# Kernel optimization log

Measured on AMD Instinct MI355X. Metric: run time of the kernel, lower is better.

The kernel has to match this reference:

```python
import jax, jax.numpy as jnp
import numpy as np
import math

D = 1024      # d_model
DC = 256      # d_cache
DL = DC // 4  # d_layer
K = 64        # num_slots
NL = 8        # num_layers
N = NL * K    # cache slots (L*K)
P = 16        # num_patterns
H = 16        # num_heads
B, S = 8, 1024
F = 4 * D

def _linear(x, w, b):
    return jnp.matmul(x, w.T) + b

def _ln(x, g, b):
    m = jnp.mean(x, -1, keepdims=True)
    v = jnp.mean((x - m) ** 2, -1, keepdims=True)
    return (x - m) * jax.lax.rsqrt(v + 1e-5) * g + b

def _mha(q, k, v, wqkv, bqkv, wo, bo, nh):
    # torch nn.MultiheadAttention (batch_first, eval/no-dropout)
    d = q.shape[-1]; dh = d // nh
    wq, wk, wv = jnp.split(wqkv, 3, axis=0)
    bq, bk, bv = jnp.split(bqkv, 3, axis=0)
    qh = _linear(q, wq, bq).reshape(q.shape[0], q.shape[1], nh, dh)
    kh = _linear(k, wk, bk).reshape(k.shape[0], k.shape[1], nh, dh)
    vh = _linear(v, wv, bv).reshape(v.shape[0], v.shape[1], nh, dh)
    s = jnp.einsum('bqhd,bkhd->bhqk', qh, kh) * (1.0 / math.sqrt(dh))
    a = jax.nn.softmax(s, axis=-1)
    o = jnp.einsum('bhqk,bkhd->bqhd', a, vh).reshape(q.shape[0], q.shape[1], d)
    return _linear(o, wo, bo)

def _forward(x, cache, slot_embeddings, layer_ids, gumbel_u, layer_embed,
             attn_wqkv, attn_bqkv, attn_wo, attn_bo,
             pat_wqkv, pat_bqkv, pat_wo, pat_bo, pattern_queries,
             ffn_w1, ffn_b1, ffn_w2, ffn_b2,
             n1_g, n1_b, n2_g, n2_b,
             gate_w, gate_b, sel_w, sel_b, sq_w, sq_b, sk_w, sk_b, an_w, an_b,
             dec_w, dec_b, cq_w, cq_b, ck_w, ck_b, cv_w, cv_b, fg_w, fg_b):
    b, s, d = x.shape
    # --- read_cache: cross-attention from tokens to [B,N,DC] cache slots ---
    cid = jnp.concatenate([cache, jnp.broadcast_to(layer_ids[None], (b,) + layer_ids.shape)], axis=-1)  # [B,N,DC+DL]
    q = _linear(x, cq_w, cq_b)                    # [B,S,DC]
    kk = _linear(cid, ck_w, ck_b)                 # [B,N,DC]
    vv = _linear(cid, cv_w, cv_b)                 # [B,N,DC]
    sc = jnp.einsum('bsd,bnd->bsn', q, kk) * (1.0 / math.sqrt(DC))
    attn = jax.nn.softmax(sc, axis=-1)
    ctx = jnp.einsum('bsn,bnd->bsd', attn, vv)    # [B,S,DC]
    ctx = jnp.concatenate([ctx, jnp.broadcast_to(layer_embed, (b, s, layer_embed.shape[-1]))], axis=-1)
    context = _linear(ctx, dec_w, dec_b)          # [B,S,D]
    # --- gated fusion ---
    gate = jax.nn.sigmoid(_linear(jnp.concatenate([x, context], axis=-1), fg_w, fg_b))
    xf = gate * x + (1.0 - gate) * context
    # --- self-attn + FFN transformer block ---
    xf = _ln(xf + _mha(xf, xf, xf, attn_wqkv, attn_bqkv, attn_wo, attn_bo, H), n1_g, n1_b)
    ffn = _linear(jax.nn.gelu(_linear(xf, ffn_w1, ffn_b1), approximate=False), ffn_w2, ffn_b2)
    y = _ln(xf + ffn, n2_g, n2_b)
    # --- pattern pooling ---
    queries = jnp.broadcast_to(pattern_queries[None], (b,) + pattern_queries.shape)
    patterns = _mha(queries, y, y, pat_wqkv, pat_bqkv, pat_wo, pat_bo, H)   # [B,P,D]
    # --- selection head (hybrid routing + gumbel-softmax, soft mode) ---
    scores = jax.nn.sigmoid(_linear(patterns, gate_w, gate_b))[..., 0]      # [B,P]
    learned = _linear(patterns, sel_w, sel_b)                               # [B,P,K]
    content = jnp.einsum('bpd,kd->bpk', _linear(patterns, sq_w, sq_b),
                         _linear(slot_embeddings, sk_w, sk_b)) * (1.0 / math.sqrt(DC))
    alpha = jax.nn.sigmoid(_linear(patterns, an_w, an_b))                   # [B,P,1]
    logits = alpha * learned + (1.0 - alpha) * content
    g = -jnp.log(-jnp.log(gumbel_u + 1e-8) + 1e-8)
    slot_probs = jax.nn.softmax(logits + g, axis=-1)  # temperature = 1.0, hard=False
    soft_probs = jax.nn.softmax(logits, axis=-1)
    return y, patterns, scores, slot_probs, soft_probs, alpha[..., 0]

def setup_inputs() -> dict:
    key = jax.random.key(0)
    ks = iter(jax.random.split(key, 64))
    def rn(shape, scale=1.0):
        return scale * jax.random.normal(next(ks), shape, dtype=jnp.float32)
    inp = {
        'x': rn((B, S, D)),
        'cache': rn((B, N, DC)),
        'slot_embeddings': rn((K, DC), 0.02),
        'layer_ids': rn((N, DL), 0.02),
        'gumbel_u': jax.random.uniform(next(ks), (B, P, K), dtype=jnp.float32, minval=1e-4, maxval=1.0),
        'layer_embed': rn((1, 1, DL), 0.02),
        'attn_wqkv': rn((3 * D, D), 0.02), 'attn_bqkv': jnp.zeros((3 * D,)),
        'attn_wo': rn((D, D), 0.02), 'attn_bo': jnp.zeros((D,)),
        'pat_wqkv': rn((3 * D, D), 0.02), 'pat_bqkv': jnp.zeros((3 * D,)),
        'pat_wo': rn((D, D), 0.02), 'pat_bo': jnp.zeros((D,)),
        'pattern_queries': rn((P, D), 0.02),
        'ffn_w1': rn((F, D), 0.02), 'ffn_b1': jnp.zeros((F,)),
        'ffn_w2': rn((D, F), 0.02), 'ffn_b2': jnp.zeros((D,)),
        'n1_g': jnp.ones((D,)), 'n1_b': jnp.zeros((D,)),
        'n2_g': jnp.ones((D,)), 'n2_b': jnp.zeros((D,)),
        'gate_w': rn((1, D), 0.02), 'gate_b': jnp.zeros((1,)),
        'sel_w': rn((K, D), 0.02), 'sel_b': jnp.zeros((K,)),
        'sq_w': rn((DC, D), 0.02), 'sq_b': jnp.zeros((DC,)),
        'sk_w': rn((DC, DC), 0.02), 'sk_b': jnp.zeros((DC,)),
        'an_w': rn((1, D), 0.02), 'an_b': jnp.zeros((1,)),
        'dec_w': rn((D, DC + DL), 0.02), 'dec_b': jnp.zeros((D,)),
        'cq_w': rn((DC, D), 0.02), 'cq_b': jnp.zeros((DC,)),
        'ck_w': rn((DC, DC + DL), 0.02), 'ck_b': jnp.zeros((DC,)),
        'cv_w': rn((DC, DC + DL), 0.02), 'cv_b': jnp.zeros((DC,)),
        'fg_w': rn((D, 2 * D), 0.02), 'fg_b': jnp.zeros((D,)),
    }
    return inp

def reference(x, cache, slot_embeddings, layer_ids, gumbel_u, layer_embed,
              attn_wqkv, attn_bqkv, attn_wo, attn_bo,
              pat_wqkv, pat_bqkv, pat_wo, pat_bo, pattern_queries,
              ffn_w1, ffn_b1, ffn_w2, ffn_b2,
              n1_g, n1_b, n2_g, n2_b,
              gate_w, gate_b, sel_w, sel_b, sq_w, sq_b, sk_w, sk_b, an_w, an_b,
              dec_w, dec_b, cq_w, cq_b, ck_w, ck_b, cv_w, cv_b, fg_w, fg_b):
    return _forward(x, cache, slot_embeddings, layer_ids, gumbel_u, layer_embed,
                    attn_wqkv, attn_bqkv, attn_wo, attn_bo,
                    pat_wqkv, pat_bqkv, pat_wo, pat_bo, pattern_queries,
                    ffn_w1, ffn_b1, ffn_w2, ffn_b2,
                    n1_g, n1_b, n2_g, n2_b,
                    gate_w, gate_b, sel_w, sel_b, sq_w, sq_b, sk_w, sk_b, an_w, an_b,
                    dec_w, dec_b, cq_w, cq_b, ck_w, ck_b, cv_w, cv_b, fg_w, fg_b)
```

## Files before the change

kernel.cpp:

```cpp
#include <hip/hip_runtime.h>
#include <math.h>

typedef unsigned short u16;
typedef unsigned int u32;
typedef __bf16 bfx8 __attribute__((ext_vector_type(8)));
typedef float fx4 __attribute__((ext_vector_type(4)));

__device__ __forceinline__ float b2f(u16 v) { return __uint_as_float(((u32)v) << 16); }
__device__ __forceinline__ u16 f2b(float f) {
    u32 u = __float_as_uint(f);
    u32 lsb = (u >> 16) & 1u;
    u += 0x7fffu + lsb;
    return (u16)(u >> 16);
}
__device__ __forceinline__ float4 unpack4(u32 a, u32 b) {
    float4 r;
    r.x = __uint_as_float(a << 16);
    r.y = __uint_as_float(a & 0xffff0000u);
    r.z = __uint_as_float(b << 16);
    r.w = __uint_as_float(b & 0xffff0000u);
    return r;
}
__device__ __forceinline__ float sigmoid_(float x) { return 1.f / (1.f + __expf(-x)); }
__device__ __forceinline__ float gelu_(float x) { return 0.5f * x * (1.f + erff(x * 0.7071067811865475f)); }

__device__ __forceinline__ float ldx(const void* p, long i, int f) {
    return f ? ((const float*)p)[i] : b2f(((const u16*)p)[i]);
}
__device__ __forceinline__ void stx(void* p, long i, float v, int f) {
    if (f) ((float*)p)[i] = v;
    else ((u16*)p)[i] = f2b(v);
}
__device__ __forceinline__ void stage8(u16* dst, const void* src, long idx, int f, bool ok) {
    uint4 r;
    if (!ok) {
        r = make_uint4(0u, 0u, 0u, 0u);
    } else if (f) {
        const float* p = (const float*)src + idx;
        float4 a = *(const float4*)p;
        float4 b = *(const float4*)(p + 4);
        r = make_uint4((u32)f2b(a.x) | ((u32)f2b(a.y) << 16),
                       (u32)f2b(a.z) | ((u32)f2b(a.w) << 16),
                       (u32)f2b(b.x) | ((u32)f2b(b.y) << 16),
                       (u32)f2b(b.z) | ((u32)f2b(b.w) << 16));
    } else {
        r = *(const uint4*)((const u16*)src + idx);
    }
    *(uint4*)dst = r;
}

__device__ __forceinline__ void glds16(const u16* g, u16* l) {
    __builtin_amdgcn_global_load_lds(
        (const __attribute__((address_space(1))) u32*)g,
        (__attribute__((address_space(3))) u32*)l, 16, 0, 0);
}

__global__ void detect_dtype(const u16* __restrict__ n1g, int* __restrict__ flag) {
    *flag = (n1g[0] == 0) ? 1 : 0;
}

__global__ __launch_bounds__(256) void conv_weights(
    const void* awqkv, const void* awo, const void* fw1, const void* fw2,
    const void* pwqkv, const void* fgw, const void* decw, const void* cqw,
    const void* ckw, const void* x, u16* __restrict__ dst, const int* __restrict__ flagp)
{
    const int f = *flagp;
    long c = ((long)blockIdx.x * 256 + threadIdx.x) * 8;
    if (c >= 25837568L) return;
    const void* src; long off;
    if      (c < 3145728L)  { src = awqkv; off = c; }
    else if (c < 4194304L)  { src = awo;   off = c - 3145728L; }
    else if (c < 8388608L)  { src = fw1;   off = c - 4194304L; }
    else if (c < 12582912L) { src = fw2;   off = c - 8388608L; }
    else if (c < 14680064L) { src = pwqkv; off = c - 12582912L + 1048576L; }
    else if (c < 16777216L) { src = fgw;   off = c - 14680064L; }
    else if (c < 17104896L) { src = decw;  off = c - 16777216L; }
    else if (c < 17367040L) { src = cqw;   off = c - 17104896L; }
    else if (c < 17448960L) { src = ckw;   off = c - 17367040L; }
    else                    { src = x;     off = c - 17448960L; }
    uint4 r;
    if (f) {
        const float* p = (const float*)src + off;
        float4 a = *(const float4*)p;
        float4 b = *(const float4*)(p + 4);
        r = make_uint4((u32)f2b(a.x) | ((u32)f2b(a.y) << 16),
                       (u32)f2b(a.z) | ((u32)f2b(a.w) << 16),
                       (u32)f2b(b.x) | ((u32)f2b(b.y) << 16),
                       (u32)f2b(b.z) | ((u32)f2b(b.w) << 16));
    } else {
        r = *(const uint4*)((const u16*)src + off);
    }
    *(uint4*)(dst + c) = r;
}

template <int ACT, int ACC>
__global__ __launch_bounds__(256) void gemm_big(
    const u16* __restrict__ A, const u16* __restrict__ B, const void* __restrict__ bias,
    u16* __restrict__ C, int M, int N, int K, int lda, int ldb, int ldc, float scale,
    long aS, long bS, long cS, long biasBase, const int* __restrict__ flagp)
{
    const int f = *flagp;
    const long z = blockIdx.z;
    const u16* Ab = A + z * aS;
    const u16* Bb = B + z * bS;
    u16* Cb = C + z * cS;

    __shared__ u16 As[8192];
    __shared__ u16 Bs[8192];

    const int tid = threadIdx.x;
    const int w = tid >> 6;
    const int lane = tid & 63;
    const int l15 = lane & 15;
    const int quad = lane >> 4;
    const int wr = w >> 1, wc = w & 1;

    const int m0 = blockIdx.y * 128;
    const int n0 = blockIdx.x * 128;

    const int srow = lane >> 3;
    const int scol = ((lane & 7) ^ srow) << 3;

    fx4 acc[4][4];
#pragma unroll
    for (int mi = 0; mi < 4; ++mi)
#pragma unroll
        for (int ni = 0; ni < 4; ++ni) {
            fx4 zz = {0.f, 0.f, 0.f, 0.f};
            acc[mi][ni] = zz;
        }

    for (int k0 = 0; k0 < K; k0 += 64) {
        __syncthreads();
#pragma unroll
        for (int j = 0; j < 4; ++j) {
            const int rg = (j * 4 + w) * 8 + srow;
            glds16(Ab + (long)(m0 + rg) * lda + k0 + scol, &As[(j * 4 + w) * 512]);
            glds16(Bb + (long)(n0 + rg) * ldb + k0 + scol, &Bs[(j * 4 + w) * 512]);
        }
        __syncthreads();
#pragma unroll
        for (int kk = 0; kk < 2; ++kk) {
            bfx8 af[4], bf[4];
#pragma unroll
            for (int i = 0; i < 4; ++i) {
                const int ar = wr * 64 + i * 16 + l15;
                af[i] = *(const bfx8*)((const char*)As + ar * 128 +
                                       ((kk * 64 + quad * 16) ^ ((ar & 7) << 4)));
                const int br = wc * 64 + i * 16 + l15;
                bf[i] = *(const bfx8*)((const char*)Bs + br * 128 +
                                       ((kk * 64 + quad * 16) ^ ((br & 7) << 4)));
            }
#pragma unroll
            for (int mi = 0; mi < 4; ++mi)
#pragma unroll
                for (int ni = 0; ni < 4; ++ni)
                    acc[mi][ni] = __builtin_amdgcn_mfma_f32_16x16x32_bf16(af[mi], bf[ni], acc[mi][ni], 0, 0, 0);
        }
    }

#pragma unroll
    for (int ni = 0; ni < 4; ++ni) {
        const int col = n0 + wc * 64 + ni * 16 + l15;
        const float bv = bias ? ldx(bias, biasBase + col, f) : 0.f;
#pragma unroll
        for (int mi = 0; mi < 4; ++mi) {
            const int row = m0 + wr * 64 + mi * 16 + quad * 4;
#pragma unroll
            for (int r = 0; r < 4; ++r) {
                float v = acc[mi][ni][r] * scale + bv;
                if (ACT) v = gelu_(v);
                long idx = (long)(row + r) * ldc + col;
                if (ACC) v += b2f(Cb[idx]);
                Cb[idx] = f2b(v);
            }
        }
    }
}

template <int OUTF32, int ACT, int TRANS, int ACC>
__global__ __launch_bounds__(256) void gemm_nt(
    const void* __restrict__ A, const void* __restrict__ B, const void* __restrict__ bias,
    void* __restrict__ Cv, int M, int N, int K, int lda, int ldb, int ldc, float scale,
    long aBase, long aDiv, long aOut, long aIn,
    long bBase, long bDiv, long bOut, long bIn,
    long cDiv, long cOut, long cIn,
    long biasBase, int aIsIn, int bIsIn, int biasIsIn, const int* __restrict__ flagp)
{
    const int dfl = *flagp;
    const int af = aIsIn ? dfl : 0;
    const int bfF = bIsIn ? dfl : 0;
    const int sf = biasIsIn ? dfl : 0;

    long bi = blockIdx.z;
    const long aOff = aBase + (bi / aDiv) * aOut + (bi % aDiv) * aIn;
    const long bOff = bBase + (bi / bDiv) * bOut + (bi % bDiv) * bIn;
    const long cOff = (bi / cDiv) * cOut + (bi % cDiv) * cIn;

    __shared__ u16 As[64][40];
    __shared__ u16 Bs[64][40];

    const int tid = threadIdx.x;
    const int w = tid >> 6;
    const int lane = tid & 63;
    const int m0 = blockIdx.y * 64;
    const int n0 = blockIdx.x * 64;

    const int lr = tid >> 2;
    const int lk = (tid & 3) * 8;

    fx4 acc[4];
#pragma unroll
    for (int c = 0; c < 4; ++c)
#pragma unroll
        for (int r = 0; r < 4; ++r) acc[c][r] = 0.f;

    const int arow = m0 + lr;
    const int brow = n0 + lr;
    const bool aok = arow < M;
    const bool bok = brow < N;

    const int row16 = lane & 15;
    const int quad = lane >> 4;

    for (int k0 = 0; k0 < K; k0 += 32) {
        __syncthreads();
        stage8(&As[lr][lk], A, aOff + (long)arow * lda + k0 + lk, af, aok);
        stage8(&Bs[lr][lk], B, bOff + (long)brow * ldb + k0 + lk, bfF, bok);
        __syncthreads();
        bfx8 afr = *(const bfx8*)&As[w * 16 + row16][quad * 8];
#pragma unroll
        for (int c = 0; c < 4; ++c) {
            bfx8 bfr = *(const bfx8*)&Bs[c * 16 + row16][quad * 8];
            acc[c] = __builtin_amdgcn_mfma_f32_16x16x32_bf16(afr, bfr, acc[c], 0, 0, 0);
        }
    }

#pragma unroll
    for (int c = 0; c < 4; ++c) {
        int col = n0 + c * 16 + row16;
        float bvv = bias ? ldx(bias, biasBase + col, sf) : 0.f;
#pragma unroll
        for (int r = 0; r < 4; ++r) {
            int row = m0 + w * 16 + quad * 4 + r;
            if (row < M) {
                float v = acc[c][r] * scale + bvv;
                if (ACT == 1) v = gelu_(v);
                long idx = TRANS ? ((long)col * ldc + row) : ((long)row * ldc + col);
                if (OUTF32) {
                    ((float*)Cv)[cOff + idx] = v;
                } else {
                    if (ACC) v += b2f(((u16*)Cv)[cOff + idx]);
                    ((u16*)Cv)[cOff + idx] = f2b(v);
                }
            }
        }
    }
}

__global__ __launch_bounds__(256) void attn_self(const u16* __restrict__ QKV, u16* __restrict__ O,
                                                 int ldo, long bStride)
{
    const int h = blockIdx.y;
    const long zoff = (long)blockIdx.z * bStride;
    const u16* Qb = QKV + zoff + h * 64;
    const u16* Kb = Qb + 1024;
    const u16* Vb = Qb + 2048;
    u16* Ob = O + zoff + h * 64;

    const int tid = threadIdx.x;
    const int w = tid >> 6;
    const int lane = tid & 63;
    const int l15 = lane & 15;
    const int quad = lane >> 4;
    const int q0 = blockIdx.x * 64;

    __shared__ u16 Ks[64][72];
    __shared__ u16 Vt[64][72];
    __shared__ u16 Ps[4][16][72];

    bfx8 aq[2];
    {
        const u16* qrow = Qb + (long)(q0 + w * 16 + l15) * 3072 + quad * 8;
        aq[0] = *(const bfx8*)(qrow);
        aq[1] = *(const bfx8*)(qrow + 32);
    }

    fx4 acc[4];
#pragma unroll
    for (int c = 0; c < 4; ++c) {
        fx4 z = {0.f, 0.f, 0.f, 0.f};
        acc[c] = z;
    }
    float m[4], l[4];
#pragma unroll
    for (int r = 0; r < 4; ++r) { m[r] = -__builtin_inff(); l[r] = 0.f; }

    const int sr = tid >> 2;
    const int sc = (tid & 3) * 16;
    const int vr = lane;
    const int vc = w * 16;

    for (int kt = 0; kt < 16; ++kt) {
        __syncthreads();
        {
            const uint4* kp = (const uint4*)(Kb + (long)(kt * 64 + sr) * 3072 + sc);
            *(uint4*)&Ks[sr][sc] = kp[0];
            *(uint4*)&Ks[sr][sc + 8] = kp[1];
        }
        {
            const u16* vp = Vb + (long)(kt * 64 + vr) * 3072 + vc;
            uint4 a = *(const uint4*)vp;
            uint4 b = *(const uint4*)(vp + 8);
            u16 tmp[16];
            *(uint4*)&tmp[0] = a;
            *(uint4*)&tmp[8] = b;
#pragma unroll
            for (int j = 0; j < 16; ++j) Vt[vc + j][vr] = tmp[j];
        }
        __syncthreads();

        fx4 s[4];
#pragma unroll
        for (int c = 0; c < 4; ++c) {
            bfx8 b0 = *(const bfx8*)&Ks[c * 16 + l15][quad * 8];
            bfx8 b1 = *(const bfx8*)&Ks[c * 16 + l15][32 + quad * 8];
            fx4 t = {0.f, 0.f, 0.f, 0.f};
            t = __builtin_amdgcn_mfma_f32_16x16x32_bf16(aq[0], b0, t, 0, 0, 0);
            t = __builtin_amdgcn_mfma_f32_16x16x32_bf16(aq[1], b1, t, 0, 0, 0);
            s[c] = t;
        }
#pragma unroll
        for (int c = 0; c < 4; ++c)
#pragma unroll
            for (int r = 0; r < 4; ++r) s[c][r] *= 0.125f;

#pragma unroll
        for (int r = 0; r < 4; ++r) {
            float tm = fmaxf(fmaxf(s[0][r], s[1][r]), fmaxf(s[2][r], s[3][r]));
#pragma unroll
            for (int off = 1; off < 16; off <<= 1) tm = fmaxf(tm, __shfl_xor(tm, off));
            float mn = fmaxf(m[r], tm);
            float al = __expf(m[r] - mn);
            m[r] = mn;
            l[r] *= al;
#pragma unroll
            for (int c = 0; c < 4; ++c) acc[c][r] *= al;
            float rs = 0.f;
#pragma unroll
            for (int c = 0; c < 4; ++c) {
                float p = __expf(s[c][r] - mn);
                s[c][r] = p;
                rs += p;
            }
#pragma unroll
            for (int off = 1; off < 16; off <<= 1) rs += __shfl_xor(rs, off);
            l[r] += rs;
        }

#pragma unroll
        for (int c = 0; c < 4; ++c)
#pragma unroll
            for (int r = 0; r < 4; ++r)
                Ps[w][quad * 4 + r][c * 16 + l15] = f2b(s[c][r]);

#pragma unroll
        for (int ks = 0; ks < 2; ++ks) {
            bfx8 ap = *(const bfx8*)&Ps[w][l15][ks * 32 + quad * 8];
#pragma unroll
            for (int c = 0; c < 4; ++c) {
                bfx8 bv = *(const bfx8*)&Vt[c * 16 + l15][ks * 32 + quad * 8];
                acc[c] = __builtin_amdgcn_mfma_f32_16x16x32_bf16(ap, bv, acc[c], 0, 0, 0);
            }
        }
    }

#pragma unroll
    for (int r = 0; r < 4; ++r) {
        float inv = 1.f / l[r];
        u16* op = Ob + (long)(q0 + w * 16 + quad * 4 + r) * ldo;
#pragma unroll
        for (int c = 0; c < 4; ++c)
            op[c * 16 + l15] = f2b(acc[c][r] * inv);
    }
}

__global__ __launch_bounds__(256) void softmax_inplace(u16* __restrict__ d, int W)
{
    long row = blockIdx.x;
    u16* r = d + row * W;
    int t = threadIdx.x;
    int n = W >> 8;
    float v[4];
    float mx = -1e30f;
    for (int i = 0; i < n; ++i) { v[i] = b2f(r[t + 256 * i]); mx = fmaxf(mx, v[i]); }
    __shared__ float red[256];
    red[t] = mx; __syncthreads();
    for (int s = 128; s > 0; s >>= 1) { if (t < s) red[t] = fmaxf(red[t], red[t + s]); __syncthreads(); }
    mx = red[0]; __syncthreads();
    float sum = 0.f;
    for (int i = 0; i < n; ++i) { v[i] = __expf(v[i] - mx); sum += v[i]; }
    red[t] = sum; __syncthreads();
    for (int s = 128; s > 0; s >>= 1) { if (t < s) red[t] += red[t + s]; __syncthreads(); }
    float inv = 1.f / red[0];
    for (int i = 0; i < n; ++i) r[t + 256 * i] = f2b(v[i] * inv);
}

__global__ __launch_bounds__(256) void add_ln(const u16* __restrict__ a, const u16* __restrict__ rres,
                                              const void* __restrict__ g, const void* __restrict__ be,
                                              u16* __restrict__ o1, void* __restrict__ o2, long o2off,
                                              const int* __restrict__ flagp)
{
    const int f = *flagp;
    long row = blockIdx.x;
    int t = threadIdx.x;
    const u16* ar = a + row * 1024;
    const u16* rr = rres + row * 1024;
    float v[4];
#pragma unroll
    for (int i = 0; i < 4; ++i) { int j = t + 256 * i; v[i] = b2f(ar[j]) + b2f(rr[j]); }
    __shared__ float red[256];
    float s = v[0] + v[1] + v[2] + v[3];
    red[t] = s; __syncthreads();
    for (int k = 128; k > 0; k >>= 1) { if (t < k) red[t] += red[t + k]; __syncthreads(); }
    float mean = red[0] * (1.f / 1024.f);
    __syncthreads();
    float sq = 0.f;
#pragma unroll
    for (int i = 0; i < 4; ++i) { float d = v[i] - mean; sq += d * d; }
    red[t] = sq; __syncthreads();
    for (int k = 128; k > 0; k >>= 1) { if (t < k) red[t] += red[t + k]; __syncthreads(); }
    float rs = rsqrtf(red[0] * (1.f / 1024.f) + 1e-5f);
#pragma unroll
    for (int i = 0; i < 4; ++i) {
        int j = t + 256 * i;
        float y = (v[i] - mean) * rs * ldx(g, j, f) + ldx(be, j, f);
        o1[row * 1024 + j] = f2b(y);
        if (o2) stx(o2, o2off + row * 1024 + j, y, f);
    }
}

__global__ __launch_bounds__(256) void build_cid(const void* __restrict__ cache, const void* __restrict__ lids,
                                                 u16* __restrict__ cid, const int* __restrict__ flagp)
{
    const int f = *flagp;
    long i = (long)blockIdx.x * 256 + threadIdx.x;
    if (i >= 4096L * 320) return;
    long row = i / 320, c = i % 320;
    float v = (c < 256) ? ldx(cache, row * 256 + c, f) : ldx(lids, (row & 511) * 64 + (c - 256), f);
    cid[i] = f2b(v);
}

__global__ __launch_bounds__(256) void fill_ctx_le(const void* __restrict__ le, u16* __restrict__ ctxcat,
                                                   const int* __restrict__ flagp)
{
    const int f = *flagp;
    long i = (long)blockIdx.x * 256 + threadIdx.x;
    if (i >= 8192L * 64) return;
    long row = i >> 6, j = i & 63;
    ctxcat[row * 320 + 256 + j] = f2b(ldx(le, j, f));
}

__global__ __launch_bounds__(256) void fusion(const void* __restrict__ x, const u16* __restrict__ ctx,
                                              u16* __restrict__ gl_xf, const int* __restrict__ flagp)
{
    const int f = *flagp;
    long i = (long)blockIdx.x * 256 + threadIdx.x;
    float gv = sigmoid_(b2f(gl_xf[i]));
    float xv = ldx(x, i, f);
    float cv = b2f(ctx[i]);
    gl_xf[i] = f2b(gv * xv + (1.f - gv) * cv);
}

__global__ __launch_bounds__(256) void cast_pat(const float* __restrict__ pf, u16* __restrict__ pb,
                                                void* __restrict__ pout, long poff,
                                                const int* __restrict__ flagp)
{
    const int f = *flagp;
    long i = (long)blockIdx.x * 256 + threadIdx.x;
    if (i >= 131072L) return;
    float v = pf[i];
    pb[i] = f2b(v);
    stx(pout, poff + i, v, f);
}

__global__ __launch_bounds__(64) void pat_pv(const u16* __restrict__ patp, const u16* __restrict__ kv,
                                             u16* __restrict__ opat, long pStride, long kvStride, long oStride)
{
    int qi = blockIdx.x, h = blockIdx.y, z = blockIdx.z, t = threadIdx.x;
    const u16* prow = patp + (long)z * pStride + ((long)(h * 16 + qi)) * 1024;
    const u16* v = kv + (long)z * kvStride + 1024 + h * 64 + t;
    float o = 0.f;
#pragma unroll 4
    for (int key = 0; key < 1024; ++key) o += b2f(prow[key]) * b2f(v[(long)key * 2048]);
    opat[(long)z * oStride + (long)qi * 1024 + h * 64 + t] = f2b(o);
}

__global__ __launch_bounds__(64) void final_head(const u16* __restrict__ patb, const float* __restrict__ learned,
                                                 const float* __restrict__ content, const void* __restrict__ gum,
                                                 const void* __restrict__ gw, const void* __restrict__ gb,
                                                 const void* __restrict__ anw, const void* __restrict__ anb,
                                                 void* __restrict__ outp, long oSC, long oSLOT, long oSOFT, long oAL,
                                                 const int* __restrict__ flagp)
{
    const int f = *flagp;
    int row = blockIdx.x;
    int t = threadIdx.x;
    float pa = 0.f, ps = 0.f;
    for (int j = t; j < 1024; j += 64) {
        float p = b2f(patb[(long)row * 1024 + j]);
        pa += p * ldx(anw, j, f);
        ps += p * ldx(gw, j, f);
    }
#pragma unroll
    for (int off = 32; off > 0; off >>= 1) { pa += __shfl_xor(pa, off); ps += __shfl_xor(ps, off); }
    float alpha = sigmoid_(pa + ldx(anb, 0, f));
    float score = sigmoid_(ps + ldx(gb, 0, f));
    float logit = alpha * learned[row * 64 + t] + (1.f - alpha) * content[row * 64 + t];
    float u = ldx(gum, row * 64 + t, f);
    float inner = -logf(u + 1e-8f) + 1e-8f;
    inner = fmaxf(inner, 1e-20f);
    float gg = -logf(inner);
    float l1 = logit + gg, l2 = logit;
    float m1 = l1, m2 = l2;
#pragma unroll
    for (int off = 32; off > 0; off >>= 1) { m1 = fmaxf(m1, __shfl_xor(m1, off)); m2 = fmaxf(m2, __shfl_xor(m2, off)); }
    float e1 = __expf(l1 - m1), e2 = __expf(l2 - m2);
    float s1 = e1, s2 = e2;
#pragma unroll
    for (int off = 32; off > 0; off >>= 1) { s1 += __shfl_xor(s1, off); s2 += __shfl_xor(s2, off); }
    stx(outp, oSLOT + row * 64 + t, e1 / s1, f);
    stx(outp, oSOFT + row * 64 + t, e2 / s2, f);
    if (t == 0) { stx(outp, oSC + row, score, f); stx(outp, oAL + row, alpha, f); }
}

static void launch_gemm(hipStream_t st, int outf32, int act, int trans, int acc,
                        const void* A, const void* B, const void* bias, void* C,
                        int M, int N, int K, int lda, int ldb, int ldc, float scale, int batch,
                        long aBase, long aD, long aO, long aI,
                        long bBase, long bD, long bO, long bI,
                        long cD, long cO, long cI,
                        long biasBase, int aIsIn, int bIsIn, int biasIsIn, const int* flagp)
{
    dim3 g(N / 64, (M + 63) / 64, batch);
#define PASS A, B, bias, C, M, N, K, lda, ldb, ldc, scale, aBase, aD, aO, aI, bBase, bD, bO, bI, \
             cD, cO, cI, biasBase, aIsIn, bIsIn, biasIsIn, flagp
    if (outf32)      gemm_nt<1, 0, 0, 0><<<g, 256, 0, st>>>(PASS);
    else if (act)    gemm_nt<0, 1, 0, 0><<<g, 256, 0, st>>>(PASS);
    else if (trans)  gemm_nt<0, 0, 1, 0><<<g, 256, 0, st>>>(PASS);
    else if (acc)    gemm_nt<0, 0, 0, 1><<<g, 256, 0, st>>>(PASS);
    else             gemm_nt<0, 0, 0, 0><<<g, 256, 0, st>>>(PASS);
#undef PASS
}

static void launch_big(hipStream_t st, int act, int acc,
                       const u16* A, const u16* B, const void* bias, u16* C,
                       int M, int N, int K, int lda, int ldb, int ldc, float scale, int batch,
                       long aS, long bS, long cS, long biasBase, const int* flagp)
{
    dim3 g(N / 128, M / 128, batch);
#define PASSB A, B, bias, C, M, N, K, lda, ldb, ldc, scale, aS, bS, cS, biasBase, flagp
    if (act)      gemm_big<1, 0><<<g, 256, 0, st>>>(PASSB);
    else if (acc) gemm_big<0, 1><<<g, 256, 0, st>>>(PASSB);
    else          gemm_big<0, 0><<<g, 256, 0, st>>>(PASSB);
#undef PASSB
}

#define WS_CID     0L
#define WS_QB      2621440L
#define WS_KKB     6815744L
#define WS_VVT     8912896L
#define WS_SC      11010048L
#define WS_CTXCAT  0L
#define WS_CONTEXT 16777216L
#define WS_XF      0L

#define CS_QKVB    33554432L
#define CS_PROJ    16777216L
#define CS_FFN1C   16777216L
#define CS_FFN2C   33554432L
#define CS_KVPATB  16777216L
#define CS_QPAT    20971520L
#define CS_PATSC   21004288L
#define CS_OPAT    21528576L
#define CS_PATF32  21790720L
#define CS_PATB    22315008L
#define CS_LEARN   22577152L
#define CS_SQP     22609920L
#define CS_SKE     22675456L
#define CS_CONT    22708224L
#define CS_FLAG    39845888L
#define CS_NEED    39845892L

#define FP_QKV     33554432L
#define FP_PROJ    16777216L
#define FP_FFN1    33554432L
#define FP_FFN2    16777216L
#define FP_KVPAT   33554432L
#define FP_PATSC   16777216L
#define FP_QPAT    100663296L
#define FP_OPAT    100696064L
#define FP_PATF32  100958208L
#define FP_PATB    101482496L
#define FP_LEARN   101744640L
#define FP_SQP     101777408L
#define FP_SKE     101842944L
#define FP_CONT    101875712L
#define FP_FLAG    101908480L
#define FP_NEED    101908484L

#define FP2_WB     102760448L
#define WB_AWQKV   0L
#define WB_AWO     3145728L
#define WB_FW1     4194304L
#define WB_FW2     8388608L
#define WB_PWKV    12582912L
#define WB_FGW     14680064L
#define WB_DECW    16777216L
#define WB_CQW     17104896L
#define WB_CKW     17367040L
#define WB_X       17448960L
#define WB_TOTAL   25837568L
#define FP2_NEED   (FP2_WB + WB_TOTAL * 2)

#define OUT_Y      0L
#define OUT_PAT    8388608L
#define OUT_SCORES 8519680L
#define OUT_SLOT   8519808L
#define OUT_SOFT   8528000L
#define OUT_ALPHA  8536192L

extern "C" void kernel_launch(void* const* d_in, const int* in_sizes, int n_in,
                              void* d_out, int out_size, void* d_ws, size_t ws_size,
                              hipStream_t stream)
{
    const void* x     = d_in[0];
    const void* cache = d_in[1];
    const void* slote = d_in[2];
    const void* lids  = d_in[3];
    const void* gum   = d_in[4];
    const void* le    = d_in[5];
    const void* awqkv = d_in[6];
    const void* abqkv = d_in[7];
    const void* awo   = d_in[8];
    const void* abo   = d_in[9];
    const void* pwqkv = d_in[10];
    const void* pbqkv = d_in[11];
    const void* pwo   = d_in[12];
    const void* pbo   = d_in[13];
    const void* pq    = d_in[14];
    const void* fw1   = d_in[15];
    const void* fb1   = d_in[16];
    const void* fw2   = d_in[17];
    const void* fb2   = d_in[18];
    const void* n1g   = d_in[19];
    const void* n1b   = d_in[20];
    const void* n2g   = d_in[21];
    const void* n2b   = d_in[22];
    const void* gw    = d_in[23];
    const void* gb    = d_in[24];
    const void* selw  = d_in[25];
    const void* selb  = d_in[26];
    const void* sqw   = d_in[27];
    const void* sqb   = d_in[28];
    const void* skw   = d_in[29];
    const void* skb   = d_in[30];
    const void* anw   = d_in[31];
    const void* anb   = d_in[32];
    const void* decw  = d_in[33];
    const void* decb  = d_in[34];
    const void* cqw   = d_in[35];
    const void* cqb   = d_in[36];
    const void* ckw   = d_in[37];
    const void* ckb   = d_in[38];
    const void* cvw   = d_in[39];
    const void* cvb   = d_in[40];
    const void* fgw   = d_in[41];
    const void* fgb   = d_in[42];

    char* ws = (char*)d_ws;
    auto W  = [&](long off) { return (u16*)(ws + off); };
    auto Wf = [&](long off) { return (float*)(ws + off); };

    const bool fast = ws_size >= (size_t)FP_NEED;
    const bool fast2 = ws_size >= (size_t)FP2_NEED;
    int* flg = (int*)(ws + (fast ? FP_FLAG : CS_FLAG));
    u16* WB = (u16*)(ws + FP2_WB);
    const long oQPAT   = fast ? FP_QPAT   : CS_QPAT;
    const long oOPAT   = fast ? FP_OPAT   : CS_OPAT;
    const long oPATF32 = fast ? FP_PATF32 : CS_PATF32;
    const long oPATB   = fast ? FP_PATB   : CS_PATB;
    const long oLEARN  = fast ? FP_LEARN  : CS_LEARN;
    const long oSQP    = fast ? FP_SQP    : CS_SQP;
    const long oSKE    = fast ? FP_SKE    : CS_SKE;
    const long oCONT   = fast ? FP_CONT   : CS_CONT;

    detect_dtype<<<1, 1, 0, stream>>>((const u16*)n1g, flg);
    if (fast2)
        conv_weights<<<12616, 256, 0, stream>>>(awqkv, awo, fw1, fw2, pwqkv, fgw, decw, cqw, ckw, x, WB, flg);
    build_cid<<<dim3((4096 * 320 + 255) / 256), 256, 0, stream>>>(cache, lids, W(WS_CID), flg);
    if (fast2)
        launch_big(stream, 0, 0, WB + WB_X, WB + WB_CQW, cqb, W(WS_QB), 8192, 256, 1024,
                   1024, 1024, 256, 1.f, 1, 0, 0, 0, 0, flg);
    else
        launch_gemm(stream, 0, 0, 0, 0, x, cqw, cqb, W(WS_QB), 8192, 256, 1024, 1024, 1024, 256, 1.f, 1,
                    0, 1, 0, 0, 0, 1, 0, 0, 1, 0, 0, 0, 1, 1, 1, flg);
    if (fast2)
        launch_big(stream, 0, 0, W(WS_CID), WB + WB_CKW, ckb, W(WS_KKB), 4096, 256, 320,
                   320, 320, 256, 1.f, 1, 0, 0, 0, 0, flg);
    else
        launch_gemm(stream, 0, 0, 0, 0, W(WS_CID), ckw, ckb, W(WS_KKB), 4096, 256, 320, 320, 320, 256, 1.f, 1,
                    0, 1, 0, 0, 0, 1, 0, 0, 1, 0, 0, 0, 0, 1, 1, flg);
    launch_gemm(stream, 0, 0, 1, 0, W(WS_CID), cvw, cvb, W(WS_VVT), 512, 256, 320, 320, 320, 512, 1.f, 8,
                0, 1, 163840, 0, 0, 1, 0, 0, 1, 131072, 0, 0, 0, 1, 1, flg);
    if (fast2)
        launch_big(stream, 0, 0, W(WS_QB), W(WS_KKB), nullptr, W(WS_SC), 1024, 512, 256,
                   256, 256, 512, 0.0625f, 8, 262144, 131072, 524288, 0, flg);
    else
        launch_gemm(stream, 0, 0, 0, 0, W(WS_QB), W(WS_KKB), nullptr, W(WS_SC), 1024, 512, 256, 256, 256, 512,
                    0.0625f, 8, 0, 1, 262144, 0, 0, 1, 131072, 0, 1, 524288, 0, 0, 0, 0, 0, flg);
    softmax_inplace<<<8192, 256, 0, stream>>>(W(WS_SC), 512);
    if (fast2)
        launch_big(stream, 0, 0, W(WS_SC), W(WS_VVT), nullptr, W(WS_CTXCAT), 1024, 256, 512,
                   512, 512, 320, 1.f, 8, 524288, 131072, 327680, 0, flg);
    else
        launch_gemm(stream, 0, 0, 0, 0, W(WS_SC), W(WS_VVT), nullptr, W(WS_CTXCAT), 1024, 256, 512, 512, 512, 320,
                    1.f, 8, 0, 1, 524288, 0, 0, 1, 131072, 0, 1, 327680, 0, 0, 0, 0, 0, flg);
    fill_ctx_le<<<dim3((8192 * 64 + 255) / 256), 256, 0, stream>>>(le, W(WS_CTXCAT), flg);
    if (fast2)
        launch_big(stream, 0, 0, W(WS_CTXCAT), WB + WB_DECW, decb, W(WS_CONTEXT), 8192, 1024, 320,
                   320, 320, 1024, 1.f, 1, 0, 0, 0, 0, flg);
    else
        launch_gemm(stream, 0, 0, 0, 0, W(WS_CTXCAT), decw, decb, W(WS_CONTEXT), 8192, 1024, 320, 320, 320, 1024,
                    1.f, 1, 0, 1, 0, 0, 0, 1, 0, 0, 1, 0, 0, 0, 0, 1, 1, flg);
    if (fast2)
        launch_big(stream, 0, 0, WB + WB_X, WB + WB_FGW, fgb, W(WS_XF), 8192, 1024, 1024,
                   1024, 2048, 1024, 1.f, 1, 0, 0, 0, 0, flg);
    else
        launch_gemm(stream, 0, 0, 0, 0, x, fgw, fgb, W(WS_XF), 8192, 1024, 1024, 1024, 2048, 1024, 1.f, 1,
                    0, 1, 0, 0, 0, 1, 0, 0, 1, 0, 0, 0, 1, 1, 1, flg);
    if (fast2)
        launch_big(stream, 0, 1, W(WS_CONTEXT), WB + WB_FGW + 1024, nullptr, W(WS_XF), 8192, 1024, 1024,
                   1024, 2048, 1024, 1.f, 1, 0, 0, 0, 0, flg);
    else
        launch_gemm(stream, 0, 0, 0, 1, W(WS_CONTEXT), fgw, nullptr, W(WS_XF), 8192, 1024, 1024, 1024, 2048, 1024,
                    1.f, 1, 0, 1, 0, 0, 1024, 1, 0, 0, 1, 0, 0, 0, 0, 1, 0, flg);
    fusion<<<32768, 256, 0, stream>>>(x, W(WS_CONTEXT), W(WS_XF), flg);

    if (fast) {
        if (fast2)
            launch_big(stream, 0, 0, W(WS_XF), WB + WB_AWQKV, abqkv, W(FP_QKV), 8192, 3072, 1024,
                       1024, 1024, 3072, 1.f, 1, 0, 0, 0, 0, flg);
        else
            launch_gemm(stream, 0, 0, 0, 0, W(WS_XF), awqkv, abqkv, W(FP_QKV), 8192, 3072, 1024,
                        1024, 1024, 3072, 1.f, 1, 0, 1, 0, 0, 0, 1, 0, 0, 1, 0, 0, 0, 0, 1, 1, flg);
        attn_self<<<dim3(16, 16, 8), 256, 0, stream>>>(W(FP_QKV), W(FP_QKV), 3072, 3145728L);
        if (fast2)
            launch_big(stream, 0, 0, W(FP_QKV), WB + WB_AWO, abo, W(FP_PROJ), 8192, 1024, 1024,
                       3072, 1024, 1024, 1.f, 1, 0, 0, 0, 0, flg);
        else
            launch_gemm(stream, 0, 0, 0, 0, W(FP_QKV), awo, abo, W(FP_PROJ), 8192, 1024, 1024,
                        3072, 1024, 1024, 1.f, 1, 0, 1, 0, 0, 0, 1, 0, 0, 1, 0, 0, 0, 0, 1, 1, flg);
        add_ln<<<8192, 256, 0, stream>>>(W(WS_XF), W(FP_PROJ), n1g, n1b, W(WS_XF), nullptr, 0, flg);
        if (fast2)
            launch_big(stream, 1, 0, W(WS_XF), WB + WB_FW1, fb1, W(FP_FFN1), 8192, 4096, 1024,
                       1024, 1024, 4096, 1.f, 1, 0, 0, 0, 0, flg);
        else
            launch_gemm(stream, 0, 1, 0, 0, W(WS_XF), fw1, fb1, W(FP_FFN1), 8192, 4096, 1024,
                        1024, 1024, 4096, 1.f, 1, 0, 1, 0, 0, 0, 1, 0, 0, 1, 0, 0, 0, 0, 1, 1, flg);
        if (fast2)
            launch_big(stream, 0, 0, W(FP_FFN1), WB + WB_FW2, fb2, W(FP_FFN2), 8192, 1024, 4096,
                       4096, 4096, 1024, 1.f, 1, 0, 0, 0, 0, flg);
        else
            launch_gemm(stream, 0, 0, 0, 0, W(FP_FFN1), fw2, fb2, W(FP_FFN2), 8192, 1024, 4096,
                        4096, 4096, 1024, 1.f, 1, 0, 1, 0, 0, 0, 1, 0, 0, 1, 0, 0, 0, 0, 1, 1, flg);
        add_ln<<<8192, 256, 0, stream>>>(W(WS_XF), W(FP_FFN2), n2g, n2b, W(WS_XF), d_out, OUT_Y, flg);
        launch_gemm(stream, 0, 0, 0, 0, pq, pwqkv, pbqkv, W(oQPAT), 16, 1024, 1024, 1024, 1024, 1024, 1.f, 1,
                    0, 1, 0, 0, 0, 1, 0, 0, 1, 0, 0, 0, 1, 1, 1, flg);
        if (fast2)
            launch_big(stream, 0, 0, W(WS_XF), WB + WB_PWKV, pbqkv, W(FP_KVPAT), 8192, 2048, 1024,
                       1024, 1024, 2048, 1.f, 1, 0, 0, 0, 1024, flg);
        else
            launch_gemm(stream, 0, 0, 0, 0, W(WS_XF), pwqkv, pbqkv, W(FP_KVPAT), 8192, 2048, 1024,
                        1024, 1024, 2048, 1.f, 1, 0, 1, 0, 0, 1048576, 1, 0, 0, 1, 0, 0, 1024, 0, 1, 1, flg);
        launch_gemm(stream, 0, 0, 0, 0, W(oQPAT), W(FP_KVPAT), nullptr, W(FP_PATSC), 16, 1024, 64,
                    1024, 2048, 1024, 0.125f, 128,
                    0, 16, 0, 64, 0, 16, 2097152, 64, 1, 16384, 0, 0, 0, 0, 0, flg);
        softmax_inplace<<<2048, 256, 0, stream>>>(W(FP_PATSC), 1024);
        pat_pv<<<dim3(16, 16, 8), 64, 0, stream>>>(W(FP_PATSC), W(FP_KVPAT), W(oOPAT),
                                                   262144L, 2097152L, 16384L);
    } else {
        for (int b = 0; b < 8; ++b) {
            launch_gemm(stream, 0, 0, 0, 0, W(WS_XF) + (long)b * 1048576, awqkv, abqkv, W(CS_QKVB),
                        1024, 3072, 1024, 1024, 1024, 3072, 1.f, 1,
                        0, 1, 0, 0, 0, 1, 0, 0, 1, 0, 0, 0, 0, 1, 1, flg);
            attn_self<<<dim3(16, 16, 1), 256, 0, stream>>>(W(CS_QKVB), W(CS_QKVB), 3072, 0L);
            launch_gemm(stream, 0, 0, 0, 0, W(CS_QKVB), awo, abo, W(CS_PROJ) + (long)b * 1048576,
                        1024, 1024, 1024, 3072, 1024, 1024, 1.f, 1,
                        0, 1, 0, 0, 0, 1, 0, 0, 1, 0, 0, 0, 0, 1, 1, flg);
        }
        add_ln<<<8192, 256, 0, stream>>>(W(WS_XF), W(CS_PROJ), n1g, n1b, W(WS_XF), nullptr, 0, flg);
        for (int c = 0; c < 4; ++c) {
            u16* xf2c = W(WS_XF) + (long)c * 2048 * 1024;
            launch_gemm(stream, 0, 1, 0, 0, xf2c, fw1, fb1, W(CS_FFN1C), 2048, 4096, 1024, 1024, 1024, 4096,
                        1.f, 1, 0, 1, 0, 0, 0, 1, 0, 0, 1, 0, 0, 0, 0, 1, 1, flg);
            launch_gemm(stream, 0, 0, 0, 0, W(CS_FFN1C), fw2, fb2, W(CS_FFN2C), 2048, 1024, 4096,
                        4096, 4096, 1024, 1.f, 1, 0, 1, 0, 0, 0, 1, 0, 0, 1, 0, 0, 0, 0, 1, 1, flg);
            add_ln<<<2048, 256, 0, stream>>>(xf2c, W(CS_FFN2C), n2g, n2b, xf2c, d_out,
                                             OUT_Y + (long)c * 2048 * 1024, flg);
        }
        launch_gemm(stream, 0, 0, 0, 0, pq, pwqkv, pbqkv, W(oQPAT), 16, 1024, 1024, 1024, 1024, 1024, 1.f, 1,
                    0, 1, 0, 0, 0, 1, 0, 0, 1, 0, 0, 0, 1, 1, 1, flg);
        for (int b = 0; b < 8; ++b) {
            const u16* yb = W(WS_XF) + (long)b * 1048576;
            launch_gemm(stream, 0, 0, 0, 0, yb, pwqkv, pbqkv, W(CS_KVPATB), 1024, 2048, 1024,
                        1024, 1024, 2048, 1.f, 1, 0, 1, 0, 0, 1048576, 1, 0, 0, 1, 0, 0, 1024, 0, 1, 1, flg);
            launch_gemm(stream, 0, 0, 0, 0, W(oQPAT), W(CS_KVPATB), nullptr, W(CS_PATSC), 16, 1024, 64,
                        1024, 2048, 1024, 0.125f, 16,
                        0, 16, 0, 64, 0, 16, 0, 64, 1, 16384, 0, 0, 0, 0, 0, flg);
            softmax_inplace<<<256, 256, 0, stream>>>(W(CS_PATSC), 1024);
            pat_pv<<<dim3(16, 16, 1), 64, 0, stream>>>(W(CS_PATSC), W(CS_KVPATB),
                                                       W(oOPAT) + (long)b * 16384, 0L, 0L, 0L);
        }
    }

    launch_gemm(stream, 1, 0, 0, 0, W(oOPAT), pwo, pbo, Wf(oPATF32), 128, 1024, 1024, 1024, 1024, 1024,
                1.f, 1, 0, 1, 0, 0, 0, 1, 0, 0, 1, 0, 0, 0, 0, 1, 1, flg);
    cast_pat<<<512, 256, 0, stream>>>(Wf(oPATF32), W(oPATB), d_out, OUT_PAT, flg);
    launch_gemm(stream, 1, 0, 0, 0, W(oPATB), selw, selb, Wf(oLEARN), 128, 64, 1024, 1024, 1024, 64,
                1.f, 1, 0, 1, 0, 0, 0, 1, 0, 0, 1, 0, 0, 0, 0, 1, 1, flg);
    launch_gemm(stream, 0, 0, 0, 0, W(oPATB), sqw, sqb, W(oSQP), 128, 256, 1024, 1024, 1024, 256, 1.f, 1,
                0, 1, 0, 0, 0, 1, 0, 0, 1, 0, 0, 0, 0, 1, 1, flg);
    launch_gemm(stream, 0, 0, 0, 0, slote, skw, skb, W(oSKE), 64, 256, 256, 256, 256, 256, 1.f, 1,
                0, 1, 0, 0, 0, 1, 0, 0, 1, 0, 0, 0, 1, 1, 1, flg);
    launch_gemm(stream, 1, 0, 0, 0, W(oSQP), W(oSKE), nullptr, Wf(oCONT), 128, 64, 256, 256, 256, 64,
                0.0625f, 1, 0, 1, 0, 0, 0, 1, 0, 0, 1, 0, 0, 0, 0, 0, 0, flg);
    final_head<<<128, 64, 0, stream>>>(W(oPATB), Wf(oLEARN), Wf(oCONT), gum, gw, gb, anw, anb,
                                       d_out, OUT_SCORES, OUT_SLOT, OUT_SOFT, OUT_ALPHA, flg);
}
```

Measured before the change: 1.199 ms.

## Double key tile to 128 and prefetch next K/V tile into registers in self-attention

```diff
diff --git a/kernel.cpp b/kernel.cpp
--- a/kernel.cpp
+++ b/kernel.cpp
@@ -275,9 +275,9 @@
     const int quad = lane >> 4;
     const int q0 = blockIdx.x * 64;
 
-    __shared__ u16 Ks[64][72];
-    __shared__ u16 Vt[64][72];
-    __shared__ u16 Ps[4][16][72];
+    __shared__ u16 Ks[128][72];
+    __shared__ u16 Vt[64][132];
+    __shared__ u16 Ps[4][16][132];
 
     bfx8 aq[2];
     {
@@ -296,33 +296,50 @@
 #pragma unroll
     for (int r = 0; r < 4; ++r) { m[r] = -__builtin_inff(); l[r] = 0.f; }
 
-    const int sr = tid >> 2;
-    const int sc = (tid & 3) * 16;
-    const int vr = lane;
-    const int vc = w * 16;
-
-    for (int kt = 0; kt < 16; ++kt) {
+    const int krow = tid >> 1;
+    const int kcol = (tid & 1) * 32;
+    const int vkey = tid & 127;
+    const int vc0 = tid >> 7;
+
+    uint4 kr[4], va[2], vb_[2];
+    auto load_tile = [&](int kt) {
+        const u16* kp = Kb + (long)(kt * 128 + krow) * 3072 + kcol;
+        kr[0] = *(const uint4*)(kp);
+        kr[1] = *(const uint4*)(kp + 8);
+        kr[2] = *(const uint4*)(kp + 16);
+        kr[3] = *(const uint4*)(kp + 24);
+        const u16* vp = Vb + (long)(kt * 128 + vkey) * 3072;
+        va[0] = *(const uint4*)(vp + vc0 * 16);
+        va[1] = *(const uint4*)(vp + vc0 * 16 + 8);
+        vb_[0] = *(const uint4*)(vp + (vc0 + 2) * 16);
+        vb_[1] = *(const uint4*)(vp + (vc0 + 2) * 16 + 8);
+    };
+
+    load_tile(0);
+
+    for (int kt = 0; kt < 8; ++kt) {
         __syncthreads();
+        *(uint4*)&Ks[krow][kcol] = kr[0];
+        *(uint4*)&Ks[krow][kcol + 8] = kr[1];
+        *(uint4*)&Ks[krow][kcol + 16] = kr[2];
+        *(uint4*)&Ks[krow][kcol + 24] = kr[3];
         {
-            const uint4* kp = (const uint4*)(Kb + (long)(kt * 64 + sr) * 3072 + sc);
-            *(uint4*)&Ks[sr][sc] = kp[0];
-            *(uint4*)&Ks[sr][sc + 8] = kp[1];
-        }
-        {
-            const u16* vp = Vb + (long)(kt * 64 + vr) * 3072 + vc;
-            uint4 a = *(const uint4*)vp;
-            uint4 b = *(const uint4*)(vp + 8);
             u16 tmp[16];
-            *(uint4*)&tmp[0] = a;
-            *(uint4*)&tmp[8] = b;
-#pragma unroll
-            for (int j = 0; j < 16; ++j) Vt[vc + j][vr] = tmp[j];
+            *(uint4*)&tmp[0] = va[0];
+            *(uint4*)&tmp[8] = va[1];
+#pragma unroll
+            for (int j = 0; j < 16; ++j) Vt[vc0 * 16 + j][vkey] = tmp[j];
+            *(uint4*)&tmp[0] = vb_[0];
+            *(uint4*)&tmp[8] = vb_[1];
+#pragma unroll
+            for (int j = 0; j < 16; ++j) Vt[(vc0 + 2) * 16 + j][vkey] = tmp[j];
         }
         __syncthreads();
-
-        fx4 s[4];
-#pragma unroll
-        for (int c = 0; c < 4; ++c) {
+        if (kt + 1 < 8) load_tile(kt + 1);
+
+        fx4 s[8];
+#pragma unroll
+        for (int c = 0; c < 8; ++c) {
             bfx8 b0 = *(const bfx8*)&Ks[c * 16 + l15][quad * 8];
             bfx8 b1 = *(const bfx8*)&Ks[c * 16 + l15][32 + quad * 8];
             fx4 t = {0.f, 0.f, 0.f, 0.f};
@@ -331,25 +348,28 @@
             s[c] = t;
         }
 #pragma unroll
-        for (int c = 0; c < 4; ++c)
+        for (int c = 0; c < 8; ++c)
 #pragma unroll
             for (int r = 0; r < 4; ++r) s[c][r] *= 0.125f;
 
 #pragma unroll
         for (int r = 0; r < 4; ++r) {
-            float tm = fmaxf(fmaxf(s[0][r], s[1][r]), fmaxf(s[2][r], s[3][r]));
+            float tm = s[0][r];
+#pragma unroll
+            for (int c = 1; c < 8; ++c) tm = fmaxf(tm, s[c][r]);
 #pragma unroll
             for (int off = 1; off < 16; off <<= 1) tm = fmaxf(tm, __shfl_xor(tm, off));
-            float mn = fmaxf(m[r], tm);
-            float al = __expf(m[r] - mn);
-            m[r] = mn;
-            l[r] *= al;
-#pragma unroll
-            for (int c = 0; c < 4; ++c) acc[c][r] *= al;
+            if (tm > m[r]) {
+                float al = __expf(m[r] - tm);
+                l[r] *= al;
+#pragma unroll
+                for (int c = 0; c < 4; ++c) acc[c][r] *= al;
+                m[r] = tm;
+            }
             float rs = 0.f;
 #pragma unroll
-            for (int c = 0; c < 4; ++c) {
-                float p = __expf(s[c][r] - mn);
+            for (int c = 0; c < 8; ++c) {
+                float p = __expf(s[c][r] - m[r]);
                 s[c][r] = p;
                 rs += p;
             }
@@ -359,13 +379,13 @@
         }
 
 #pragma unroll
-        for (int c = 0; c < 4; ++c)
+        for (int c = 0; c < 8; ++c)
 #pragma unroll
             for (int r = 0; r < 4; ++r)
                 Ps[w][quad * 4 + r][c * 16 + l15] = f2b(s[c][r]);
 
 #pragma unroll
-        for (int ks = 0; ks < 2; ++ks) {
+        for (int ks = 0; ks < 4; ++ks) {
             bfx8 ap = *(const bfx8*)&Ps[w][l15][ks * 32 + quad * 8];
 #pragma unroll
             for (int c = 0; c < 4; ++c) {
```

Result: slower. 1.234 ms (+3.0%).
